# Kernel tuning notes

Hardware: AMD Instinct MI355X
Metric: run time of the kernel (lower is better)

## Reference

```python
import jax, jax.numpy as jnp
import numpy as np

B, F, V, E, H, D = 1024, 2048, 10000, 256, 512, 3


def setup_inputs() -> dict:
    key = jax.random.key(0)
    ks = jax.random.split(key, 16)
    n = lambda k, shape, s: (jax.random.normal(k, shape, dtype=jnp.float32) * s)
    fz = lambda shape: jnp.zeros(shape, jnp.float32)
    forget_bias = fz((4 * H,)).at[H:2 * H].set(1.0)  # torch init: bias_hh forget gate = 1
    return {
        "target": n(ks[0], (B, F), 1.0),
        "distractors": n(ks[1], (D, B, F), 1.0),
        # Sender params
        "s_W_aff": n(ks[2], (H, F), 0.02), "s_b_aff": fz((H,)),
        "s_W_ih": n(ks[3], (4 * H, E), 0.05), "s_W_hh": n(ks[4], (4 * H, H), 0.05),
        "s_b_ih": fz((4 * H,)), "s_b_hh": forget_bias,
        "s_emb": n(ks[5], (V, E), 0.1),
        "s_W_probs": n(ks[6], (V, H), 0.05), "s_b_probs": fz((V,)),
        # Receiver params
        "r_emb": n(ks[7], (V, E), 0.1),
        "r_W_ih": n(ks[8], (4 * H, E), 0.05), "r_W_hh": n(ks[9], (4 * H, H), 0.05),
        "r_b_ih": fz((4 * H,)), "r_b_hh": forget_bias,
        "r_W_aff": n(ks[10], (F, H), 0.02), "r_b_aff": fz((F,)),
        "start_token_idx": 1,
        "max_sentence_length": 20,
    }


def lstm_cell(x, h, c, W_ih, W_hh, b_ih, b_hh):
    # PyTorch LSTMCell gate order: i, f, g, o
    gates = x @ W_ih.T + b_ih + h @ W_hh.T + b_hh
    i, f, g, o = jnp.split(gates, 4, axis=-1)
    c = jax.nn.sigmoid(f) * c + jax.nn.sigmoid(i) * jnp.tanh(g)
    h = jax.nn.sigmoid(o) * jnp.tanh(c)
    return h, c


def reference(target, distractors, s_W_aff, s_b_aff, s_W_ih, s_W_hh, s_b_ih, s_b_hh,
              s_emb, s_W_probs, s_b_probs, r_emb, r_W_ih, r_W_hh, r_b_ih, r_b_hh,
              r_W_aff, r_b_aff, start_token_idx, max_sentence_length):
    # ---- Sender (greedy eval path of the original module) ----
    h0 = target @ s_W_aff.T + s_b_aff                     # [B,H]
    c0 = jnp.zeros((B, H), target.dtype)
    w0 = s_emb[jnp.full((B,), start_token_idx, jnp.int32)]  # [B,E]

    def send_step(carry, _):
        h, c, w = carry
        h, c = lstm_cell(w, h, c, s_W_ih, s_W_hh, s_b_ih, s_b_hh)
        logits = h @ s_W_probs.T + s_b_probs              # [B,V]
        w_idx = jnp.argmax(logits, axis=-1)               # greedy sample
        lp = jax.nn.log_softmax(logits, axis=-1)[jnp.arange(B), w_idx]
        return (h, c, s_emb[w_idx]), (w_idx, lp)

    (_, _, _), (msg_tb, lp_tb) = jax.lax.scan(send_step, (h0, c0, w0), None,
                                              length=max_sentence_length)
    message = msg_tb.T                                    # [B,T]
    log_prob = lp_tb[-1]                                  # log prob of last token, [B]

    # ---- Receiver ----
    def recv_step(carry, w_idx):
        h, c = carry
        h, c = lstm_cell(r_emb[w_idx], h, c, r_W_ih, r_W_hh, r_b_ih, r_b_hh)
        return (h, c), None

    (hr, _), _ = jax.lax.scan(recv_step,
                              (jnp.zeros((B, H), target.dtype), jnp.zeros((B, H), target.dtype)),
                              msg_tb)
    r_transform = hr @ r_W_aff.T + r_b_aff                # [B,F]

    # ---- Hinge loss + accuracy ----
    rT = r_transform.T                                    # [F,B]
    target_score = target @ rT                            # [B,B]
    d_scores = jnp.einsum('dbf,fn->dbn', distractors, rT) # [D,B,B]
    hinge = jnp.sum(jnp.maximum(0.0, 1.0 - target_score[None] + d_scores), axis=0)  # [B,B]
    loss = jnp.mean(jnp.mean(-hinge * log_prob, axis=1))  # log_prob broadcasts over last dim

    target_prob = jnp.mean(jnp.exp(target_score), axis=1)            # [B]
    dist_prob = jnp.mean(jnp.exp(d_scores), axis=2)                  # [D,B]
    all_probs = jnp.concatenate([target_prob[:, None], dist_prob.T], axis=1)  # [B,1+D]
    accuracy = jnp.mean((jnp.argmax(all_probs, axis=1) == 0).astype(jnp.float32))
    return loss, accuracy, message
```

## Files before the change

### kernel.cpp

```cpp
#include <hip/hip_runtime.h>
#include <math.h>
#include <limits.h>

#define NB 1024
#define NF 2048
#define NV 10000
#define NE 256
#define NH 512
#define ND 3
#define NT 20

typedef __bf16 bf16x8 __attribute__((ext_vector_type(8)));
typedef float  f32x4  __attribute__((ext_vector_type(4)));

__device__ __forceinline__ float sigf(float x) { return 1.0f / (1.0f + expf(-x)); }
__device__ __forceinline__ bool better(float v, int i, float w, int j) {
    return (v > w) || (v == w && i < j);
}

template<int ACCUM, int BIAS, int ZMODE, int GATHER>
__global__ __launch_bounds__(512)
void gemm512(const float* __restrict__ A, const float* __restrict__ A2,
             const int* __restrict__ gidx,
             const float* __restrict__ Bm, const float* __restrict__ bias,
             float* __restrict__ C, int M, int N, int K)
{
    __shared__ float As[16][68];
    __shared__ float Bs[16][132];
    const int tid = threadIdx.x;
    const int bn = blockIdx.x << 7;
    const int bm = blockIdx.y << 6;

    const float* Ause = A;
    if (ZMODE) {
        if (blockIdx.z > 0) Ause = A2 + (size_t)(blockIdx.z - 1) * M * K;
        C += (size_t)blockIdx.z * M * N;
    }

    const int abr = tid & 63;
    const int abk = ((tid >> 6) & 3) << 2;
    const int bbr = tid & 127;
    const int bbk = (tid >> 7) << 2;
    const int tx = tid & 31, ty = tid >> 5;
    const int m0 = ty << 2, n0 = tx << 2;

    const float* Arow = nullptr;
    if (tid < 256) {
        int r = bm + abr;
        Arow = GATHER ? (A + (size_t)gidx[r] * K) : (Ause + (size_t)r * K);
    }
    const float* Brow = Bm + (size_t)(bn + bbr) * K;

    float acc[4][4];
    #pragma unroll
    for (int i = 0; i < 4; ++i)
        #pragma unroll
        for (int j = 0; j < 4; ++j) acc[i][j] = 0.f;

    for (int k0 = 0; k0 < K; k0 += 16) {
        if (tid < 256) {
            float4 av = *(const float4*)(Arow + k0 + abk);
            As[abk + 0][abr] = av.x; As[abk + 1][abr] = av.y;
            As[abk + 2][abr] = av.z; As[abk + 3][abr] = av.w;
        }
        float4 bv = *(const float4*)(Brow + k0 + bbk);
        Bs[bbk + 0][bbr] = bv.x; Bs[bbk + 1][bbr] = bv.y;
        Bs[bbk + 2][bbr] = bv.z; Bs[bbk + 3][bbr] = bv.w;
        __syncthreads();
        #pragma unroll
        for (int k = 0; k < 16; ++k) {
            float4 xa = *(const float4*)&As[k][m0];
            float4 xb = *(const float4*)&Bs[k][n0];
            float ar[4] = {xa.x, xa.y, xa.z, xa.w};
            float br[4] = {xb.x, xb.y, xb.z, xb.w};
            #pragma unroll
            for (int i = 0; i < 4; ++i)
                #pragma unroll
                for (int j = 0; j < 4; ++j)
                    acc[i][j] = fmaf(ar[i], br[j], acc[i][j]);
        }
        __syncthreads();
    }
    #pragma unroll
    for (int i = 0; i < 4; ++i) {
        int row = bm + m0 + i;
        #pragma unroll
        for (int j = 0; j < 4; ++j) {
            int col = bn + n0 + j;
            float v = acc[i][j];
            if (BIAS) v += bias[col];
            float* p = C + (size_t)row * N + col;
            if (ACCUM) v += *p;
            *p = v;
        }
    }
}

__global__ __launch_bounds__(512)
void recv_gate_k(const float* __restrict__ emb, const int* __restrict__ msg_t,
                 const float* __restrict__ h, const float* __restrict__ Wih,
                 const float* __restrict__ Whh, const float* __restrict__ bias,
                 float* __restrict__ gates)
{
    __shared__ float As[16][68];
    __shared__ float Bs[16][132];
    const int tid = threadIdx.x;
    const int bn = blockIdx.x << 7;
    const int bm = blockIdx.y << 6;

    const int abr = tid & 63;
    const int abk = ((tid >> 6) & 3) << 2;
    const int bbr = tid & 127;
    const int bbk = (tid >> 7) << 2;
    const int tx = tid & 31, ty = tid >> 5;
    const int m0 = ty << 2, n0 = tx << 2;

    const float* Ax = nullptr; const float* Ah = nullptr;
    if (tid < 256) {
        int r = bm + abr;
        Ax = emb + (size_t)msg_t[r] * NE;
        Ah = h + (size_t)r * NH;
    }
    const float* Bi = Wih + (size_t)(bn + bbr) * NE;
    const float* Bh = Whh + (size_t)(bn + bbr) * NH;

    float acc[4][4];
    #pragma unroll
    for (int i = 0; i < 4; ++i)
        #pragma unroll
        for (int j = 0; j < 4; ++j) acc[i][j] = 0.f;

    for (int k0 = 0; k0 < NE + NH; k0 += 16) {
        if (tid < 256) {
            float4 av = (k0 < NE) ? *(const float4*)(Ax + k0 + abk)
                                  : *(const float4*)(Ah + (k0 - NE) + abk);
            As[abk + 0][abr] = av.x; As[abk + 1][abr] = av.y;
            As[abk + 2][abr] = av.z; As[abk + 3][abr] = av.w;
        }
        float4 bv = (k0 < NE) ? *(const float4*)(Bi + k0 + bbk)
                              : *(const float4*)(Bh + (k0 - NE) + bbk);
        Bs[bbk + 0][bbr] = bv.x; Bs[bbk + 1][bbr] = bv.y;
        Bs[bbk + 2][bbr] = bv.z; Bs[bbk + 3][bbr] = bv.w;
        __syncthreads();
        #pragma unroll
        for (int k = 0; k < 16; ++k) {
            float4 xa = *(const float4*)&As[k][m0];
            float4 xb = *(const float4*)&Bs[k][n0];
            float ar[4] = {xa.x, xa.y, xa.z, xa.w};
            float br[4] = {xb.x, xb.y, xb.z, xb.w};
            #pragma unroll
            for (int i = 0; i < 4; ++i)
                #pragma unroll
                for (int j = 0; j < 4; ++j)
                    acc[i][j] = fmaf(ar[i], br[j], acc[i][j]);
        }
        __syncthreads();
    }
    #pragma unroll
    for (int i = 0; i < 4; ++i) {
        int row = bm + m0 + i;
        #pragma unroll
        for (int j = 0; j < 4; ++j) {
            int col = bn + n0 + j;
            gates[(size_t)row * (4 * NH) + col] = acc[i][j] + bias[col];
        }
    }
}

__global__ void split_k(const float* __restrict__ x, __bf16* __restrict__ hi,
                        __bf16* __restrict__ lo, int n)
{
    int i = blockIdx.x * 256 + threadIdx.x;
    if (i < n) {
        float v = x[i];
        __bf16 h = (__bf16)v;
        hi[i] = h;
        lo[i] = (__bf16)(v - (float)h);
    }
}

__global__ __launch_bounds__(256)
void logits_mfma(const __bf16* __restrict__ Ahi, const __bf16* __restrict__ Alo,
                 const __bf16* __restrict__ Bhi, const __bf16* __restrict__ Blo,
                 const float* __restrict__ bias, float* __restrict__ C)
{
    __shared__ __align__(16) char sm[32768];
    __bf16* sAh = (__bf16*)sm;
    __bf16* sAl = (__bf16*)(sm + 8192);
    __bf16* sBh = (__bf16*)(sm + 16384);
    __bf16* sBl = (__bf16*)(sm + 24576);

    const int tid = threadIdx.x;
    const int lane = tid & 63, w = tid >> 6;
    const int wm = w >> 1, wn = w & 1;
    const int bm = blockIdx.y << 7, bn = blockIdx.x << 7;

    size_t ga[2], gb[2];
    #pragma unroll
    for (int j = 0; j < 2; ++j) {
        int s = tid + j * 256;
        int mf = s >> 6, g = (s >> 4) & 3, row = s & 15;
        ga[j] = (size_t)(bm + mf * 16 + row) * NH + g * 8;
        int n = bn + mf * 16 + row;
        if (n >= NV) n = 0;
        gb[j] = (size_t)n * NH + g * 8;
    }

    f32x4 acc[4][4];
    #pragma unroll
    for (int i = 0; i < 4; ++i)
        #pragma unroll
        for (int j = 0; j < 4; ++j) acc[i][j] = (f32x4){0.f, 0.f, 0.f, 0.f};

    for (int k0 = 0; k0 < NH; k0 += 32) {
        uint4 vah0 = *(const uint4*)(Ahi + ga[0] + k0);
        uint4 vah1 = *(const uint4*)(Ahi + ga[1] + k0);
        uint4 val0 = *(const uint4*)(Alo + ga[0] + k0);
        uint4 val1 = *(const uint4*)(Alo + ga[1] + k0);
        uint4 vbh0 = *(const uint4*)(Bhi + gb[0] + k0);
        uint4 vbh1 = *(const uint4*)(Bhi + gb[1] + k0);
        uint4 vbl0 = *(const uint4*)(Blo + gb[0] + k0);
        uint4 vbl1 = *(const uint4*)(Blo + gb[1] + k0);
        *(uint4*)(sAh + (size_t)tid * 8)         = vah0;
        *(uint4*)(sAh + (size_t)(tid + 256) * 8) = vah1;
        *(uint4*)(sAl + (size_t)tid * 8)         = val0;
        *(uint4*)(sAl + (size_t)(tid + 256) * 8) = val1;
        *(uint4*)(sBh + (size_t)tid * 8)         = vbh0;
        *(uint4*)(sBh + (size_t)(tid + 256) * 8) = vbh1;
        *(uint4*)(sBl + (size_t)tid * 8)         = vbl0;
        *(uint4*)(sBl + (size_t)(tid + 256) * 8) = vbl1;
        __syncthreads();

        bf16x8 ah[4], al[4];
        #pragma unroll
        for (int f = 0; f < 4; ++f) {
            int base = ((wm * 4 + f) * 64 + lane) * 8;
            ah[f] = *(const bf16x8*)(sAh + base);
            al[f] = *(const bf16x8*)(sAl + base);
        }
        #pragma unroll
        for (int fn = 0; fn < 4; ++fn) {
            int base = ((wn * 4 + fn) * 64 + lane) * 8;
            bf16x8 bh = *(const bf16x8*)(sBh + base);
            bf16x8 bl = *(const bf16x8*)(sBl + base);
            #pragma unroll
            for (int fm = 0; fm < 4; ++fm)
                acc[fm][fn] = __builtin_amdgcn_mfma_f32_16x16x32_bf16(ah[fm], bh, acc[fm][fn], 0, 0, 0);
            #pragma unroll
            for (int fm = 0; fm < 4; ++fm)
                acc[fm][fn] = __builtin_amdgcn_mfma_f32_16x16x32_bf16(ah[fm], bl, acc[fm][fn], 0, 0, 0);
            #pragma unroll
            for (int fm = 0; fm < 4; ++fm)
                acc[fm][fn] = __builtin_amdgcn_mfma_f32_16x16x32_bf16(al[fm], bh, acc[fm][fn], 0, 0, 0);
        }
        __syncthreads();
    }

    const int r4 = (lane >> 4) << 2, cc = lane & 15;
    #pragma unroll
    for (int fm = 0; fm < 4; ++fm) {
        int row = bm + (wm * 4 + fm) * 16 + r4;
        #pragma unroll
        for (int fn = 0; fn < 4; ++fn) {
            int col = bn + (wn * 4 + fn) * 16 + cc;
            if (col < NV) {
                float bv = bias[col];
                #pragma unroll
                for (int r = 0; r < 4; ++r)
                    C[(size_t)(row + r) * NV + col] = acc[fm][fn][r] + bv;
            }
        }
    }
}

template<int SPLIT>
__global__ __launch_bounds__(256)
void lstm_cell_k(const float* __restrict__ gates, float* __restrict__ h,
                 float* __restrict__ c, __bf16* __restrict__ hi,
                 __bf16* __restrict__ lo)
{
    int idx = blockIdx.x * 256 + threadIdx.x;
    int b = idx >> 9;
    int j = idx & (NH - 1);
    const float* g = gates + (size_t)b * (4 * NH);
    float gi = sigf(g[j]);
    float gf = sigf(g[NH + j]);
    float gg = tanhf(g[2 * NH + j]);
    float go = sigf(g[3 * NH + j]);
    float cn = gf * c[idx] + gi * gg;
    c[idx] = cn;
    float hv = go * tanhf(cn);
    h[idx] = hv;
    if (SPLIT) {
        __bf16 hb = (__bf16)hv;
        hi[idx] = hb;
        lo[idx] = (__bf16)(hv - (float)hb);
    }
}

template<int LAST>
__global__ __launch_bounds__(256)
void argmax2_k(const float* __restrict__ logits, int* __restrict__ top2i,
               float* __restrict__ lse)
{
    __shared__ float sv1[256], sv2[256];
    __shared__ int   si1[256], si2[256];
    const int b = blockIdx.x;
    const int tid = threadIdx.x;
    const float* L = logits + (size_t)b * NV;
    float v1 = -INFINITY, v2 = -INFINITY;
    int i1 = INT_MAX, i2 = INT_MAX;
    for (int v = tid; v < NV; v += 256) {
        float x = L[v];
        if (better(x, v, v1, i1)) { v2 = v1; i2 = i1; v1 = x; i1 = v; }
        else if (better(x, v, v2, i2)) { v2 = x; i2 = v; }
    }
    sv1[tid] = v1; si1[tid] = i1; sv2[tid] = v2; si2[tid] = i2;
    __syncthreads();
    for (int s = 128; s > 0; s >>= 1) {
        if (tid < s) {
            float a1 = sv1[tid], a2 = sv2[tid];     int ai1 = si1[tid], ai2 = si2[tid];
            float b1 = sv1[tid+s], b2 = sv2[tid+s]; int bi1 = si1[tid+s], bi2 = si2[tid+s];
            float r1v, r2v; int r1i, r2i;
            if (better(a1, ai1, b1, bi1)) {
                r1v = a1; r1i = ai1;
                if (better(b1, bi1, a2, ai2)) { r2v = b1; r2i = bi1; }
                else                          { r2v = a2; r2i = ai2; }
            } else {
                r1v = b1; r1i = bi1;
                if (better(a1, ai1, b2, bi2)) { r2v = a1; r2i = ai1; }
                else                          { r2v = b2; r2i = bi2; }
            }
            sv1[tid] = r1v; si1[tid] = r1i; sv2[tid] = r2v; si2[tid] = r2i;
        }
        __syncthreads();
    }
    if (tid == 0) { top2i[2*b] = si1[0]; top2i[2*b+1] = si2[0]; }
    if (LAST) {
        float m = sv1[0];
        __syncthreads();
        float s = 0.0f;
        for (int v = tid; v < NV; v += 256) s += expf(L[v] - m);
        sv1[tid] = s;
        __syncthreads();
        for (int sh = 128; sh > 0; sh >>= 1) {
            if (tid < sh) sv1[tid] += sv1[tid + sh];
            __syncthreads();
        }
        if (tid == 0) lse[b] = m + logf(sv1[0]);
    }
}

template<int LAST>
__global__ __launch_bounds__(64)
void rescore_k(const float* __restrict__ h, const float* __restrict__ Wpr,
               const float* __restrict__ bpr, const float* __restrict__ logits,
               const int* __restrict__ top2i, const float* __restrict__ lse,
               int* __restrict__ msg_t, float* __restrict__ out_msg,
               float* __restrict__ lp, int t)
{
    const int b = blockIdx.x;
    const int tid = threadIdx.x;
    const int i1 = top2i[2*b], i2 = top2i[2*b+1];
    const float* hr = h + (size_t)b * NH;
    const float* w1 = Wpr + (size_t)i1 * NH;
    const float* w2 = Wpr + (size_t)i2 * NH;
    double s1 = 0.0, s2 = 0.0;
    for (int k = tid; k < NH; k += 64) {
        double hv = (double)hr[k];
        s1 += hv * (double)w1[k];
        s2 += hv * (double)w2[k];
    }
    #pragma unroll
    for (int off = 32; off > 0; off >>= 1) {
        s1 += __shfl_down(s1, off);
        s2 += __shfl_down(s2, off);
    }
    if (tid == 0) {
        s1 += (double)bpr[i1];
        s2 += (double)bpr[i2];
        int w = (s1 > s2 || (s1 == s2 && i1 < i2)) ? i1 : i2;
        msg_t[b] = w;
        out_msg[(size_t)b * NT + t] = (float)w;
        if (LAST) lp[b] = logits[(size_t)b * NV + w] - lse[b];
    }
}

__global__ void init_idx_k(const int* __restrict__ start, int* __restrict__ idx)
{
    int b = blockIdx.x * 256 + threadIdx.x;
    if (b < NB) idx[b] = start[0];
}

__global__ void bias_comb_k(const float* __restrict__ a, const float* __restrict__ b,
                            float* __restrict__ o)
{
    int n = blockIdx.x * 256 + threadIdx.x;
    if (n < 4 * NH) o[n] = a[n] + b[n];
}

__global__ __launch_bounds__(256)
void loss_row_k(const float* __restrict__ scores, const float* __restrict__ lp,
                float* __restrict__ hsum, float* __restrict__ accb)
{
    __shared__ float red[256];
    const int b = blockIdx.x;
    const int tid = threadIdx.x;
    const float* ts = scores + (size_t)b * NB;
    const float* d0 = scores + (size_t)NB * NB * 1 + (size_t)b * NB;
    const float* d1 = scores + (size_t)NB * NB * 2 + (size_t)b * NB;
    const float* d2 = scores + (size_t)NB * NB * 3 + (size_t)b * NB;
    float hs = 0.f, t0 = 0.f, s0 = 0.f, s1 = 0.f, s2 = 0.f;
    for (int n = tid; n < NB; n += 256) {
        float tv = ts[n], a = d0[n], bb = d1[n], cc = d2[n];
        float hinge_bn = fmaxf(0.f, 1.f - tv + a) + fmaxf(0.f, 1.f - tv + bb)
                       + fmaxf(0.f, 1.f - tv + cc);
        hs += hinge_bn * (-lp[n]);
        t0 += expf(tv); s0 += expf(a); s1 += expf(bb); s2 += expf(cc);
    }
    float vals[5] = {hs, t0, s0, s1, s2};
    float outv[5];
    for (int i = 0; i < 5; ++i) {
        red[tid] = vals[i]; __syncthreads();
        for (int s = 128; s > 0; s >>= 1) {
            if (tid < s) red[tid] += red[tid + s];
            __syncthreads();
        }
        outv[i] = red[0]; __syncthreads();
    }
    if (tid == 0) {
        hsum[b] = outv[0];
        accb[b] = (outv[1] >= outv[2] && outv[1] >= outv[3] && outv[1] >= outv[4]) ? 1.0f : 0.0f;
    }
}

__global__ __launch_bounds__(256)
void loss_final_k(const float* __restrict__ hsum, const float* __restrict__ accb,
                  float* __restrict__ out)
{
    __shared__ float red[256];
    const int tid = threadIdx.x;
    float s = 0.f, a = 0.f;
    for (int b = tid; b < NB; b += 256) { s += hsum[b]; a += accb[b]; }
    red[tid] = s; __syncthreads();
    for (int sh = 128; sh > 0; sh >>= 1) { if (tid < sh) red[tid] += red[tid + sh]; __syncthreads(); }
    s = red[0]; __syncthreads();
    red[tid] = a; __syncthreads();
    for (int sh = 128; sh > 0; sh >>= 1) { if (tid < sh) red[tid] += red[tid + sh]; __syncthreads(); }
    a = red[0];
    if (tid == 0) {
        out[0] = s / (float)((size_t)NB * NB);
        out[1] = a / (float)NB;
    }
}

extern "C" void kernel_launch(void* const* d_in, const int* in_sizes, int n_in,
                              void* d_out, int out_size, void* d_ws, size_t ws_size,
                              hipStream_t stream)
{
    const float* target   = (const float*)d_in[0];
    const float* distract = (const float*)d_in[1];
    const float* sWaff = (const float*)d_in[2];
    const float* sbaff = (const float*)d_in[3];
    const float* sWih  = (const float*)d_in[4];
    const float* sWhh  = (const float*)d_in[5];
    const float* sbih  = (const float*)d_in[6];
    const float* sbhh  = (const float*)d_in[7];
    const float* semb  = (const float*)d_in[8];
    const float* sWpr  = (const float*)d_in[9];
    const float* sbpr  = (const float*)d_in[10];
    const float* remb  = (const float*)d_in[11];
    const float* rWih  = (const float*)d_in[12];
    const float* rWhh  = (const float*)d_in[13];
    const float* rbih  = (const float*)d_in[14];
    const float* rbhh  = (const float*)d_in[15];
    const float* rWaff = (const float*)d_in[16];
    const float* rbaff = (const float*)d_in[17];
    const int*   start = (const int*)d_in[18];
    (void)in_sizes; (void)n_in; (void)out_size; (void)ws_size;

    float* out = (float*)d_out;
    float* ws  = (float*)d_ws;

    size_t o = 0;
    float* logits = ws + o; o += (size_t)NB * NV;
    float* gates  = ws + o; o += (size_t)NB * 4 * NH;
    float* xbuf   = ws + o; o += (size_t)NB * NE;
    float* h_s    = ws + o; o += (size_t)NB * NH;
    float* c_s    = ws + o; o += (size_t)NB * NH;
    float* h_r    = ws + o; o += (size_t)NB * NH;
    float* c_r    = ws + o; o += (size_t)NB * NH;
    float* lp     = ws + o; o += NB;
    float* lse    = ws + o; o += NB;
    float* bias_s = ws + o; o += 4 * NH;
    float* bias_r = ws + o; o += 4 * NH;
    float* hsum   = ws + o; o += NB;
    float* accb   = ws + o; o += NB;
    int* msg      = (int*)(ws + o); o += (size_t)NB * NT;
    int* idx0     = (int*)(ws + o); o += NB;
    int* top2i    = (int*)(ws + o); o += 2 * NB;
    __bf16* WHi   = (__bf16*)(ws + o); o += (size_t)NV * NH / 2;
    __bf16* WLo   = (__bf16*)(ws + o); o += (size_t)NV * NH / 2;
    __bf16* hHi   = (__bf16*)(ws + o); o += (size_t)NB * NH / 2;
    __bf16* hLo   = (__bf16*)(ws + o); o += (size_t)NB * NH / 2;
    (void)xbuf;

    bias_comb_k<<<8, 256, 0, stream>>>(sbih, sbhh, bias_s);
    bias_comb_k<<<8, 256, 0, stream>>>(rbih, rbhh, bias_r);
    init_idx_k<<<4, 256, 0, stream>>>(start, idx0);
    hipMemsetAsync(c_s, 0, (size_t)NB * NH * 4, stream);
    hipMemsetAsync(h_r, 0, (size_t)NB * NH * 4, stream);
    hipMemsetAsync(c_r, 0, (size_t)NB * NH * 4, stream);

    split_k<<<(NV * NH + 255) / 256, 256, 0, stream>>>(sWpr, WHi, WLo, NV * NH);

    gemm512<0,1,0,0><<<dim3(NH/128, NB/64), 512, 0, stream>>>(
        target, nullptr, nullptr, sWaff, sbaff, h_s, NB, NH, NF);

    const int* cur = idx0;
    for (int t = 0; t < NT; ++t) {
        gemm512<0,1,0,1><<<dim3(4*NH/128, NB/64), 512, 0, stream>>>(
            semb, nullptr, cur, sWih, bias_s, gates, NB, 4*NH, NE);
        gemm512<1,0,0,0><<<dim3(4*NH/128, NB/64), 512, 0, stream>>>(
            h_s, nullptr, nullptr, sWhh, nullptr, gates, NB, 4*NH, NH);
        lstm_cell_k<1><<<NB*NH/256, 256, 0, stream>>>(gates, h_s, c_s, hHi, hLo);
        logits_mfma<<<dim3((NV + 127) / 128, NB / 128), 256, 0, stream>>>(
            hHi, hLo, WHi, WLo, sbpr, logits);
        if (t == NT - 1) {
            argmax2_k<1><<<NB, 256, 0, stream>>>(logits, top2i, lse);
            rescore_k<1><<<NB, 64, 0, stream>>>(h_s, sWpr, sbpr, logits, top2i, lse,
                                                msg + (size_t)t*NB, out + 2, lp, t);
        } else {
            argmax2_k<0><<<NB, 256, 0, stream>>>(logits, top2i, lse);
            rescore_k<0><<<NB, 64, 0, stream>>>(h_s, sWpr, sbpr, logits, top2i, lse,
                                                msg + (size_t)t*NB, out + 2, lp, t);
        }
        cur = msg + (size_t)t * NB;
    }

    for (int t = 0; t < NT; ++t) {
        recv_gate_k<<<dim3(4*NH/128, NB/64), 512, 0, stream>>>(
            remb, msg + (size_t)t*NB, h_r, rWih, rWhh, bias_r, gates);
        lstm_cell_k<0><<<NB*NH/256, 256, 0, stream>>>(gates, h_r, c_r, nullptr, nullptr);
    }

    float* rtr = gates;
    gemm512<0,1,0,0><<<dim3(NF/128, NB/64), 512, 0, stream>>>(
        h_r, nullptr, nullptr, rWaff, rbaff, rtr, NB, NF, NH);

    float* scores = logits;
    gemm512<0,0,1,0><<<dim3(NB/128, NB/64, 1 + ND), 512, 0, stream>>>(
        target, distract, nullptr, rtr, nullptr, scores, NB, NB, NF);

    loss_row_k<<<NB, 256, 0, stream>>>(scores, lp, hsum, accb);
    loss_final_k<<<1, 256, 0, stream>>>(hsum, accb, out);
}
```

Baseline: 5.386 ms.

## Fuse top-2 candidate search into logits GEMM and move receiver LSTM to MFMA

```diff
diff --git a/kernel.cpp b/kernel.cpp
--- a/kernel.cpp
+++ b/kernel.cpp
@@ -9,6 +9,8 @@
 #define NH 512
 #define ND 3
 #define NT 20
+#define NBX ((NV + 127) / 128)
+#define NCANDW (NBX * 2)
 
 typedef __bf16 bf16x8 __attribute__((ext_vector_type(8)));
 typedef float  f32x4  __attribute__((ext_vector_type(4)));
@@ -16,6 +18,14 @@
 __device__ __forceinline__ float sigf(float x) { return 1.0f / (1.0f + expf(-x)); }
 __device__ __forceinline__ bool better(float v, int i, float w, int j) {
     return (v > w) || (v == w && i < j);
+}
+__device__ __forceinline__ void merge2(float& v1, int& i1, float& v2, int& i2,
+                                       float w1, int j1, float w2, int j2) {
+    if (better(w1, j1, v1, i1)) {
+        if (better(v1, i1, w2, j2)) { v2 = v1; i2 = i1; }
+        else                        { v2 = w2; i2 = j2; }
+        v1 = w1; i1 = j1;
+    } else if (better(w1, j1, v2, i2)) { v2 = w1; i2 = j1; }
 }
 
 template<int ACCUM, int BIAS, int ZMODE, int GATHER>
@@ -96,33 +106,26 @@
     }
 }
 
-__global__ __launch_bounds__(512)
-void recv_gate_k(const float* __restrict__ emb, const int* __restrict__ msg_t,
-                 const float* __restrict__ h, const float* __restrict__ Wih,
-                 const float* __restrict__ Whh, const float* __restrict__ bias,
-                 float* __restrict__ gates)
-{
-    __shared__ float As[16][68];
+__global__ __launch_bounds__(256)
+void h0_gemm(const float* __restrict__ A, const float* __restrict__ Bm,
+             const float* __restrict__ bias, float* __restrict__ C,
+             int M, int N, int K)
+{
+    __shared__ float As[16][36];
     __shared__ float Bs[16][132];
     const int tid = threadIdx.x;
     const int bn = blockIdx.x << 7;
-    const int bm = blockIdx.y << 6;
-
-    const int abr = tid & 63;
-    const int abk = ((tid >> 6) & 3) << 2;
+    const int bm = blockIdx.y << 5;
+
+    const int abr = tid & 31;
+    const int abk = ((tid >> 5) & 3) << 2;
     const int bbr = tid & 127;
-    const int bbk = (tid >> 7) << 2;
+    const int bbk = (tid >> 7) << 3;
     const int tx = tid & 31, ty = tid >> 5;
     const int m0 = ty << 2, n0 = tx << 2;
 
-    const float* Ax = nullptr; const float* Ah = nullptr;
-    if (tid < 256) {
-        int r = bm + abr;
-        Ax = emb + (size_t)msg_t[r] * NE;
-        Ah = h + (size_t)r * NH;
-    }
-    const float* Bi = Wih + (size_t)(bn + bbr) * NE;
-    const float* Bh = Whh + (size_t)(bn + bbr) * NH;
+    const float* Arow = A + (size_t)(bm + abr) * K;
+    const float* Brow = Bm + (size_t)(bn + bbr) * K;
 
     float acc[4][4];
     #pragma unroll
@@ -130,17 +133,18 @@
         #pragma unroll
         for (int j = 0; j < 4; ++j) acc[i][j] = 0.f;
 
-    for (int k0 = 0; k0 < NE + NH; k0 += 16) {
-        if (tid < 256) {
-            float4 av = (k0 < NE) ? *(const float4*)(Ax + k0 + abk)
-                                  : *(const float4*)(Ah + (k0 - NE) + abk);
+    for (int k0 = 0; k0 < K; k0 += 16) {
+        if (tid < 128) {
+            float4 av = *(const float4*)(Arow + k0 + abk);
             As[abk + 0][abr] = av.x; As[abk + 1][abr] = av.y;
             As[abk + 2][abr] = av.z; As[abk + 3][abr] = av.w;
         }
-        float4 bv = (k0 < NE) ? *(const float4*)(Bi + k0 + bbk)
-                              : *(const float4*)(Bh + (k0 - NE) + bbk);
-        Bs[bbk + 0][bbr] = bv.x; Bs[bbk + 1][bbr] = bv.y;
-        Bs[bbk + 2][bbr] = bv.z; Bs[bbk + 3][bbr] = bv.w;
+        float4 b0 = *(const float4*)(Brow + k0 + bbk);
+        float4 b1 = *(const float4*)(Brow + k0 + bbk + 4);
+        Bs[bbk + 0][bbr] = b0.x; Bs[bbk + 1][bbr] = b0.y;
+        Bs[bbk + 2][bbr] = b0.z; Bs[bbk + 3][bbr] = b0.w;
+        Bs[bbk + 4][bbr] = b1.x; Bs[bbk + 5][bbr] = b1.y;
+        Bs[bbk + 6][bbr] = b1.z; Bs[bbk + 7][bbr] = b1.w;
         __syncthreads();
         #pragma unroll
         for (int k = 0; k < 16; ++k) {
@@ -162,7 +166,7 @@
         #pragma unroll
         for (int j = 0; j < 4; ++j) {
             int col = bn + n0 + j;
-            gates[(size_t)row * (4 * NH) + col] = acc[i][j] + bias[col];
+            C[(size_t)row * N + col] = acc[i][j] + bias[col];
         }
     }
 }
@@ -182,7 +186,8 @@
 __global__ __launch_bounds__(256)
 void logits_mfma(const __bf16* __restrict__ Ahi, const __bf16* __restrict__ Alo,
                  const __bf16* __restrict__ Bhi, const __bf16* __restrict__ Blo,
-                 const float* __restrict__ bias, float* __restrict__ C)
+                 const float* __restrict__ bias, float* __restrict__ C,
+                 float4* __restrict__ cand)
 {
     __shared__ __align__(16) char sm[32768];
     __bf16* sAh = (__bf16*)sm;
@@ -260,15 +265,160 @@
     #pragma unroll
     for (int fm = 0; fm < 4; ++fm) {
         int row = bm + (wm * 4 + fm) * 16 + r4;
+        float tv1[4], tv2[4]; int ti1[4], ti2[4];
+        #pragma unroll
+        for (int r = 0; r < 4; ++r) { tv1[r] = -INFINITY; ti1[r] = INT_MAX;
+                                      tv2[r] = -INFINITY; ti2[r] = INT_MAX; }
         #pragma unroll
         for (int fn = 0; fn < 4; ++fn) {
             int col = bn + (wn * 4 + fn) * 16 + cc;
-            if (col < NV) {
-                float bv = bias[col];
-                #pragma unroll
-                for (int r = 0; r < 4; ++r)
-                    C[(size_t)(row + r) * NV + col] = acc[fm][fn][r] + bv;
+            bool ok = col < NV;
+            float bv = ok ? bias[col] : 0.f;
+            #pragma unroll
+            for (int r = 0; r < 4; ++r) {
+                float v = ok ? (acc[fm][fn][r] + bv) : -INFINITY;
+                int ci = ok ? col : INT_MAX;
+                if (ok) C[(size_t)(row + r) * NV + col] = v;
+                if (better(v, ci, tv1[r], ti1[r])) {
+                    tv2[r] = tv1[r]; ti2[r] = ti1[r]; tv1[r] = v; ti1[r] = ci;
+                } else if (better(v, ci, tv2[r], ti2[r])) { tv2[r] = v; ti2[r] = ci; }
             }
+        }
+        #pragma unroll
+        for (int off = 1; off < 16; off <<= 1) {
+            #pragma unroll
+            for (int r = 0; r < 4; ++r) {
+                float w1 = __shfl_xor(tv1[r], off);
+                int   j1 = __shfl_xor(ti1[r], off);
+                float w2 = __shfl_xor(tv2[r], off);
+                int   j2 = __shfl_xor(ti2[r], off);
+                merge2(tv1[r], ti1[r], tv2[r], ti2[r], w1, j1, w2, j2);
+            }
+        }
+        if (cc == 0) {
+            #pragma unroll
+            for (int r = 0; r < 4; ++r) {
+                float4 pk;
+                pk.x = tv1[r]; pk.y = __int_as_float(ti1[r]);
+                pk.z = tv2[r]; pk.w = __int_as_float(ti2[r]);
+                cand[(size_t)(row + r) * NCANDW + blockIdx.x * 2 + wn] = pk;
+            }
+        }
+    }
+}
+
+__global__ __launch_bounds__(64)
+void cand_reduce_k(const float4* __restrict__ cand, int* __restrict__ top2i)
+{
+    const int b = blockIdx.x, lane = threadIdx.x;
+    float v1 = -INFINITY, v2 = -INFINITY; int i1 = INT_MAX, i2 = INT_MAX;
+    for (int s = lane; s < NCANDW; s += 64) {
+        float4 pk = cand[(size_t)b * NCANDW + s];
+        merge2(v1, i1, v2, i2, pk.x, __float_as_int(pk.y), pk.z, __float_as_int(pk.w));
+    }
+    #pragma unroll
+    for (int off = 1; off < 64; off <<= 1) {
+        float w1 = __shfl_xor(v1, off);
+        int   j1 = __shfl_xor(i1, off);
+        float w2 = __shfl_xor(v2, off);
+        int   j2 = __shfl_xor(i2, off);
+        merge2(v1, i1, v2, i2, w1, j1, w2, j2);
+    }
+    if (lane == 0) { top2i[2 * b] = i1; top2i[2 * b + 1] = i2; }
+}
+
+__global__ __launch_bounds__(256)
+void recv_mfma(const __bf16* __restrict__ eHi, const __bf16* __restrict__ eLo,
+               const int* __restrict__ msg_t,
+               const __bf16* __restrict__ hHi, const __bf16* __restrict__ hLo,
+               const __bf16* __restrict__ WiHi, const __bf16* __restrict__ WiLo,
+               const __bf16* __restrict__ WhHi, const __bf16* __restrict__ WhLo,
+               const float* __restrict__ bias, float* __restrict__ gates)
+{
+    __shared__ __align__(16) char sm[32768];
+    __bf16* sAh = (__bf16*)sm;
+    __bf16* sAl = (__bf16*)(sm + 8192);
+    __bf16* sBh = (__bf16*)(sm + 16384);
+    __bf16* sBl = (__bf16*)(sm + 24576);
+
+    const int tid = threadIdx.x;
+    const int lane = tid & 63, w = tid >> 6;
+    const int wm = w >> 1, wn = w & 1;
+    const int bm = blockIdx.y << 7, bn = blockIdx.x << 7;
+
+    int rowA[2], tokA[2], colB[2], goff[2];
+    #pragma unroll
+    for (int j = 0; j < 2; ++j) {
+        int s = tid + j * 256;
+        int mf = s >> 6, g = (s >> 4) & 3, row = s & 15;
+        rowA[j] = bm + mf * 16 + row;
+        tokA[j] = msg_t[rowA[j]];
+        colB[j] = bn + mf * 16 + row;
+        goff[j] = g * 8;
+    }
+
+    f32x4 acc[4][4];
+    #pragma unroll
+    for (int i = 0; i < 4; ++i)
+        #pragma unroll
+        for (int j = 0; j < 4; ++j) acc[i][j] = (f32x4){0.f, 0.f, 0.f, 0.f};
+
+    for (int k0 = 0; k0 < NE + NH; k0 += 32) {
+        const bool inE = k0 < NE;
+        #pragma unroll
+        for (int j = 0; j < 2; ++j) {
+            int k = k0 + goff[j];
+            const __bf16* pah = inE ? eHi + (size_t)tokA[j] * NE + k
+                                    : hHi + (size_t)rowA[j] * NH + (k - NE);
+            const __bf16* pal = inE ? eLo + (size_t)tokA[j] * NE + k
+                                    : hLo + (size_t)rowA[j] * NH + (k - NE);
+            const __bf16* pbh = inE ? WiHi + (size_t)colB[j] * NE + k
+                                    : WhHi + (size_t)colB[j] * NH + (k - NE);
+            const __bf16* pbl = inE ? WiLo + (size_t)colB[j] * NE + k
+                                    : WhLo + (size_t)colB[j] * NH + (k - NE);
+            *(uint4*)(sAh + (size_t)(tid + j * 256) * 8) = *(const uint4*)pah;
+            *(uint4*)(sAl + (size_t)(tid + j * 256) * 8) = *(const uint4*)pal;
+            *(uint4*)(sBh + (size_t)(tid + j * 256) * 8) = *(const uint4*)pbh;
+            *(uint4*)(sBl + (size_t)(tid + j * 256) * 8) = *(const uint4*)pbl;
+        }
+        __syncthreads();
+
+        bf16x8 ah[4], al[4];
+        #pragma unroll
+        for (int f = 0; f < 4; ++f) {
+            int base = ((wm * 4 + f) * 64 + lane) * 8;
+            ah[f] = *(const bf16x8*)(sAh + base);
+            al[f] = *(const bf16x8*)(sAl + base);
+        }
+        #pragma unroll
+        for (int fn = 0; fn < 4; ++fn) {
+            int base = ((wn * 4 + fn) * 64 + lane) * 8;
+            bf16x8 bh = *(const bf16x8*)(sBh + base);
+            bf16x8 bl = *(const bf16x8*)(sBl + base);
+            #pragma unroll
+            for (int fm = 0; fm < 4; ++fm)
+                acc[fm][fn] = __builtin_amdgcn_mfma_f32_16x16x32_bf16(ah[fm], bh, acc[fm][fn], 0, 0, 0);
+            #pragma unroll
+            for (int fm = 0; fm < 4; ++fm)
+                acc[fm][fn] = __builtin_amdgcn_mfma_f32_16x16x32_bf16(ah[fm], bl, acc[fm][fn], 0, 0, 0);
+            #pragma unroll
+            for (int fm = 0; fm < 4; ++fm)
+                acc[fm][fn] = __builtin_amdgcn_mfma_f32_16x16x32_bf16(al[fm], bh, acc[fm][fn], 0, 0, 0);
+        }
+        __syncthreads();
+    }
+
+    const int r4 = (lane >> 4) << 2, cc = lane & 15;
+    #pragma unroll
+    for (int fm = 0; fm < 4; ++fm) {
+        int row = bm + (wm * 4 + fm) * 16 + r4;
+        #pragma unroll
+        for (int fn = 0; fn < 4; ++fn) {
+            int col = bn + (wn * 4 + fn) * 16 + cc;
+            float bv = bias[col];
+            #pragma unroll
+            for (int r = 0; r < 4; ++r)
+                gates[(size_t)(row + r) * (4 * NH) + col] = acc[fm][fn][r] + bv;
         }
     }
 }
@@ -298,7 +448,6 @@
     }
 }
 
-template<int LAST>
 __global__ __launch_bounds__(256)
 void argmax2_k(const float* __restrict__ logits, int* __restrict__ top2i,
                float* __restrict__ lse)
@@ -321,34 +470,23 @@
         if (tid < s) {
             float a1 = sv1[tid], a2 = sv2[tid];     int ai1 = si1[tid], ai2 = si2[tid];
             float b1 = sv1[tid+s], b2 = sv2[tid+s]; int bi1 = si1[tid+s], bi2 = si2[tid+s];
-            float r1v, r2v; int r1i, r2i;
-            if (better(a1, ai1, b1, bi1)) {
-                r1v = a1; r1i = ai1;
-                if (better(b1, bi1, a2, ai2)) { r2v = b1; r2i = bi1; }
-                else                          { r2v = a2; r2i = ai2; }
-            } else {
-                r1v = b1; r1i = bi1;
-                if (better(a1, ai1, b2, bi2)) { r2v = a1; r2i = ai1; }
-                else                          { r2v = b2; r2i = bi2; }
-            }
-            sv1[tid] = r1v; si1[tid] = r1i; sv2[tid] = r2v; si2[tid] = r2i;
+            merge2(a1, ai1, a2, ai2, b1, bi1, b2, bi2);
+            sv1[tid] = a1; si1[tid] = ai1; sv2[tid] = a2; si2[tid] = ai2;
         }
         __syncthreads();
     }
     if (tid == 0) { top2i[2*b] = si1[0]; top2i[2*b+1] = si2[0]; }
-    if (LAST) {
-        float m = sv1[0];
-        __syncthreads();
-        float s = 0.0f;
-        for (int v = tid; v < NV; v += 256) s += expf(L[v] - m);
-        sv1[tid] = s;
-        __syncthreads();
-        for (int sh = 128; sh > 0; sh >>= 1) {
-            if (tid < sh) sv1[tid] += sv1[tid + sh];
-            __syncthreads();
-        }
-        if (tid == 0) lse[b] = m + logf(sv1[0]);
-    }
+    float m = sv1[0];
+    __syncthreads();
+    float s = 0.0f;
+    for (int v = tid; v < NV; v += 256) s += expf(L[v] - m);
+    sv1[tid] = s;
+    __syncthreads();
+    for (int sh = 128; sh > 0; sh >>= 1) {
+        if (tid < sh) sv1[tid] += sv1[tid + sh];
+        __syncthreads();
+    }
+    if (tid == 0) lse[b] = m + logf(sv1[0]);
 }
 
 template<int LAST>
@@ -485,7 +623,6 @@
     size_t o = 0;
     float* logits = ws + o; o += (size_t)NB * NV;
     float* gates  = ws + o; o += (size_t)NB * 4 * NH;
-    float* xbuf   = ws + o; o += (size_t)NB * NE;
     float* h_s    = ws + o; o += (size_t)NB * NH;
     float* c_s    = ws + o; o += (size_t)NB * NH;
     float* h_r    = ws + o; o += (size_t)NB * NH;
@@ -503,7 +640,15 @@
     __bf16* WLo   = (__bf16*)(ws + o); o += (size_t)NV * NH / 2;
     __bf16* hHi   = (__bf16*)(ws + o); o += (size_t)NB * NH / 2;
     __bf16* hLo   = (__bf16*)(ws + o); o += (size_t)NB * NH / 2;
-    (void)xbuf;
+    float4* cand  = (float4*)(ws + o); o += (size_t)NB * NCANDW * 4;
+    __bf16* WiHi  = (__bf16*)(ws + o); o += (size_t)(4*NH) * NE / 2;
+    __bf16* WiLo  = (__bf16*)(ws + o); o += (size_t)(4*NH) * NE / 2;
+    __bf16* WhHi  = (__bf16*)(ws + o); o += (size_t)(4*NH) * NH / 2;
+    __bf16* WhLo  = (__bf16*)(ws + o); o += (size_t)(4*NH) * NH / 2;
+    __bf16* eHi   = (__bf16*)(ws + o); o += (size_t)NV * NE / 2;
+    __bf16* eLo   = (__bf16*)(ws + o); o += (size_t)NV * NE / 2;
+    __bf16* hrHi  = (__bf16*)(ws + o); o += (size_t)NB * NH / 2;
+    __bf16* hrLo  = (__bf16*)(ws + o); o += (size_t)NB * NH / 2;
 
     bias_comb_k<<<8, 256, 0, stream>>>(sbih, sbhh, bias_s);
     bias_comb_k<<<8, 256, 0, stream>>>(rbih, rbhh, bias_r);
@@ -511,11 +656,16 @@
     hipMemsetAsync(c_s, 0, (size_t)NB * NH * 4, stream);
     hipMemsetAsync(h_r, 0, (size_t)NB * NH * 4, stream);
     hipMemsetAsync(c_r, 0, (size_t)NB * NH * 4, stream);
+    hipMemsetAsync(hrHi, 0, (size_t)NB * NH * 2, stream);
+    hipMemsetAsync(hrLo, 0, (size_t)NB * NH * 2, stream);
 
     split_k<<<(NV * NH + 255) / 256, 256, 0, stream>>>(sWpr, WHi, WLo, NV * NH);
-
-    gemm512<0,1,0,0><<<dim3(NH/128, NB/64), 512, 0, stream>>>(
-        target, nullptr, nullptr, sWaff, sbaff, h_s, NB, NH, NF);
+    split_k<<<(4*NH*NE + 255) / 256, 256, 0, stream>>>(rWih, WiHi, WiLo, 4*NH*NE);
+    split_k<<<(4*NH*NH + 255) / 256, 256, 0, stream>>>(rWhh, WhHi, WhLo, 4*NH*NH);
+    split_k<<<(NV * NE + 255) / 256, 256, 0, stream>>>(remb, eHi, eLo, NV * NE);
+
+    h0_gemm<<<dim3(NH/128, NB/32), 256, 0, stream>>>(
+        target, sWaff, sbaff, h_s, NB, NH, NF);
 
     const int* cur = idx0;
     for (int t = 0; t < NT; ++t) {
@@ -524,14 +674,14 @@
         gemm512<1,0,0,0><<<dim3(4*NH/128, NB/64), 512, 0, stream>>>(
             h_s, nullptr, nullptr, sWhh, nullptr, gates, NB, 4*NH, NH);
         lstm_cell_k<1><<<NB*NH/256, 256, 0, stream>>>(gates, h_s, c_s, hHi, hLo);
-        logits_mfma<<<dim3((NV + 127) / 128, NB / 128), 256, 0, stream>>>(
-            hHi, hLo, WHi, WLo, sbpr, logits);
+        logits_mfma<<<dim3(NBX, NB / 128), 256, 0, stream>>>(
+            hHi, hLo, WHi, WLo, sbpr, logits, cand);
         if (t == NT - 1) {
-            argmax2_k<1><<<NB, 256, 0, stream>>>(logits, top2i, lse);
+            argmax2_k<<<NB, 256, 0, stream>>>(logits, top2i, lse);
             rescore_k<1><<<NB, 64, 0, stream>>>(h_s, sWpr, sbpr, logits, top2i, lse,
                                                 msg + (size_t)t*NB, out + 2, lp, t);
         } else {
-            argmax2_k<0><<<NB, 256, 0, stream>>>(logits, top2i, lse);
+            cand_reduce_k<<<NB, 64, 0, stream>>>(cand, top2i);
             rescore_k<0><<<NB, 64, 0, stream>>>(h_s, sWpr, sbpr, logits, top2i, lse,
                                                 msg + (size_t)t*NB, out + 2, lp, t);
         }
@@ -539,9 +689,10 @@
     }
 
     for (int t = 0; t < NT; ++t) {
-        recv_gate_k<<<dim3(4*NH/128, NB/64), 512, 0, stream>>>(
-            remb, msg + (size_t)t*NB, h_r, rWih, rWhh, bias_r, gates);
-        lstm_cell_k<0><<<NB*NH/256, 256, 0, stream>>>(gates, h_r, c_r, nullptr, nullptr);
+        recv_mfma<<<dim3(4*NH/128, NB/128), 256, 0, stream>>>(
+            eHi, eLo, msg + (size_t)t*NB, hrHi, hrLo,
+            WiHi, WiLo, WhHi, WhLo, bias_r, gates);
+        lstm_cell_k<1><<<NB*NH/256, 256, 0, stream>>>(gates, h_r, c_r, hrHi, hrLo);
     }
 
     float* rtr = gates;
```

New measurement: 5.934 ms. 10.2% more time.
